# Performance work log

Measured on AMD Instinct MI355X. Metric: run time of the kernel, lower is better.

Reference implementation:

```python
import jax, jax.numpy as jnp
import numpy as np

D_MODEL = 1024
NUM_HEADS = 16
HEAD_DIM = D_MODEL // NUM_HEADS
ROPE_BASE = 10000.0


def setup_inputs() -> dict:
    key = jax.random.key(0)
    ks = jax.random.split(key, 9)
    B, S = 2, 2048
    x = jax.random.normal(ks[0], (B, S, D_MODEL), dtype=jnp.float32)
    s = 1.0 / np.sqrt(D_MODEL)
    Wq = jax.random.normal(ks[1], (D_MODEL, D_MODEL), dtype=jnp.float32) * s
    bq = jnp.zeros((D_MODEL,), dtype=jnp.float32)
    Wk = jax.random.normal(ks[2], (D_MODEL, D_MODEL), dtype=jnp.float32) * s
    bk = jnp.zeros((D_MODEL,), dtype=jnp.float32)
    Wv = jax.random.normal(ks[3], (D_MODEL, D_MODEL), dtype=jnp.float32) * s
    bv = jnp.zeros((D_MODEL,), dtype=jnp.float32)
    Wo = jax.random.normal(ks[4], (D_MODEL, D_MODEL), dtype=jnp.float32) * s
    bo = jnp.zeros((D_MODEL,), dtype=jnp.float32)
    return {"x": x, "Wq": Wq, "bq": bq, "Wk": Wk, "bk": bk,
            "Wv": Wv, "bv": bv, "Wo": Wo, "bo": bo}


def _apply_rope(x):
    # x: [B, H, S, Dh]; interleaved complex-pair RoPE (torch.view_as_complex style)
    B, H, S, Dh = x.shape
    inv_freq = 1.0 / (ROPE_BASE ** (jnp.arange(0, Dh, 2, dtype=jnp.float32) / Dh))
    pos = jnp.arange(S, dtype=jnp.float32)
    freqs = pos[:, None] * inv_freq[None, :]            # [S, Dh/2]
    cos, sin = jnp.cos(freqs), jnp.sin(freqs)           # each [S, Dh/2]
    x2 = x.reshape(B, H, S, Dh // 2, 2)
    xr, xi = x2[..., 0], x2[..., 1]
    out_r = xr * cos - xi * sin
    out_i = xr * sin + xi * cos
    return jnp.stack([out_r, out_i], axis=-1).reshape(B, H, S, Dh)


def reference(x, Wq, bq, Wk, bk, Wv, bv, Wo, bo):
    B, S, _ = x.shape
    H, Dh = NUM_HEADS, HEAD_DIM
    def proj(W, b):
        y = jnp.einsum('bsd,ed->bse', x, W) + b          # torch Linear: x @ W.T + b
        return y.reshape(B, S, H, Dh).transpose(0, 2, 1, 3)  # [B,H,S,Dh]
    Q = _apply_rope(proj(Wq, bq))
    K = _apply_rope(proj(Wk, bk))
    V = proj(Wv, bv)
    scale = 1.0 / jnp.sqrt(jnp.float32(Dh))
    scores = jnp.einsum('bhqd,bhkd->bhqk', Q, K) * scale
    causal = jnp.tril(jnp.ones((S, S), dtype=bool))
    scores = jnp.where(causal, scores, jnp.float32(-jnp.inf))
    attn = jax.nn.softmax(scores, axis=-1)
    out = jnp.einsum('bhqk,bhkd->bhqd', attn, V)         # [B,H,S,Dh]
    out = out.transpose(0, 2, 1, 3).reshape(B, S, H * Dh)
    return jnp.einsum('bsd,ed->bse', out, Wo) + bo
```

## Files before the change

### kernel.cpp

```cpp
#include <hip/hip_runtime.h>
#include <stdint.h>

#define S_LEN 2048
#define BATCH 2
#define DM 1024
#define NH 16
#define DH 64
#define MROWS 4096

typedef unsigned short u16;
typedef unsigned int u32;
typedef __attribute__((ext_vector_type(8))) short bf16x8;
typedef __attribute__((ext_vector_type(4))) short bf16x4;
typedef __attribute__((ext_vector_type(4))) float f32x4;
typedef __attribute__((ext_vector_type(2))) unsigned u32x2;

union pack8 { u32 w[4]; bf16x8 v8; };

__device__ inline u16 f2bf(float f) {
  union { float f; unsigned u; } v; v.f = f;
  unsigned u = v.u;
  unsigned r = u + 0x7fffu + ((u >> 16) & 1u);
  return (u16)(r >> 16);
}

__device__ inline u32 pkbf(float lo, float hi) {
  u32 r;
  asm("v_cvt_pk_bf16_f32 %0, %1, %2" : "=v"(r) : "v"(lo), "v"(hi));
  return r;
}

__global__ void convert_k(const float* __restrict__ x, const float* __restrict__ wq,
                          const float* __restrict__ wk, const float* __restrict__ wv,
                          const float* __restrict__ wo, u16* __restrict__ xb,
                          u16* __restrict__ wb) {
  int i = blockIdx.x * blockDim.x + threadIdx.x;
  const int total = (MROWS * DM + 4 * DM * DM) / 4;
  if (i >= total) return;
  int e = i * 4;
  const float* src;
  u16* dst;
  if (e < MROWS * DM) {
    src = x + e; dst = xb + e;
  } else {
    int j = e - MROWS * DM;
    int w = j >> 20;
    int o = j & ((1 << 20) - 1);
    src = (w == 0) ? wq + o : (w == 1) ? wk + o : (w == 2) ? wv + o : wo + o;
    dst = wb + j;
  }
  float4 v = *(const float4*)src;
  uint2 r;
  r.x = (unsigned)f2bf(v.x) | ((unsigned)f2bf(v.y) << 16);
  r.y = (unsigned)f2bf(v.z) | ((unsigned)f2bf(v.w) << 16);
  *(uint2*)dst = r;
}

__global__ void rope_k(float2* __restrict__ tab) {
  int i = blockIdx.x * blockDim.x + threadIdx.x;
  if (i >= S_LEN * 32) return;
  int s = i >> 5, p = i & 31;
  float inv = expf(-(float)p * 0.28782313662425575f);
  float a = (float)s * inv;
  tab[i] = make_float2(cosf(a), sinf(a));
}

__launch_bounds__(256)
__global__ void gemm_k(const u16* __restrict__ A,
                       const u16* __restrict__ w0, const u16* __restrict__ w1,
                       const u16* __restrict__ w2,
                       const float* __restrict__ b0, const float* __restrict__ b1,
                       const float* __restrict__ b2,
                       const float2* __restrict__ rope,
                       void* __restrict__ o0, void* __restrict__ o1, void* __restrict__ o2,
                       int mode0) {
  const int mode = mode0 + (int)(blockIdx.x >> 8);
  const int tile = blockIdx.x & 255;
  const int mt = tile >> 3, nt = tile & 7;
  const int mbase = mt * 128, nbase = nt * 128;
  const u16* W = (mode == 1) ? w1 : (mode == 2) ? w2 : w0;
  const float* bias = (mode == 1) ? b1 : (mode == 2) ? b2 : b0;
  void* outp = (mode == 1) ? o1 : (mode == 2) ? o2 : o0;

  __shared__ u16 As[128 * 40];
  __shared__ u16 Bs[128 * 40];

  const int t = threadIdx.x;
  const int lane = t & 63, wvi = t >> 6;
  const int lr = lane & 15, lg = lane >> 4;
  const int wm = (wvi >> 1) * 64, wn = (wvi & 1) * 64;

  f32x4 acc[4][4] = {};
  const int srow = t >> 2;
  const int scol = (t & 3) * 8;

  for (int kk = 0; kk < DM; kk += 32) {
    bf16x8 a0 = *(const bf16x8*)(A + (size_t)(mbase + srow) * DM + kk + scol);
    bf16x8 a1 = *(const bf16x8*)(A + (size_t)(mbase + 64 + srow) * DM + kk + scol);
    bf16x8 g0 = *(const bf16x8*)(W + (size_t)(nbase + srow) * DM + kk + scol);
    bf16x8 g1 = *(const bf16x8*)(W + (size_t)(nbase + 64 + srow) * DM + kk + scol);
    __syncthreads();
    *(bf16x8*)&As[srow * 40 + scol] = a0;
    *(bf16x8*)&As[(64 + srow) * 40 + scol] = a1;
    *(bf16x8*)&Bs[srow * 40 + scol] = g0;
    *(bf16x8*)&Bs[(64 + srow) * 40 + scol] = g1;
    __syncthreads();
    bf16x8 af[4], bfr[4];
#pragma unroll
    for (int mi = 0; mi < 4; mi++)
      af[mi] = *(const bf16x8*)&As[(wm + mi * 16 + lr) * 40 + lg * 8];
#pragma unroll
    for (int ni = 0; ni < 4; ni++)
      bfr[ni] = *(const bf16x8*)&Bs[(wn + ni * 16 + lr) * 40 + lg * 8];
#pragma unroll
    for (int mi = 0; mi < 4; mi++)
#pragma unroll
      for (int ni = 0; ni < 4; ni++)
        acc[mi][ni] = __builtin_amdgcn_mfma_f32_16x16x32_bf16(af[mi], bfr[ni], acc[mi][ni], 0, 0, 0);
  }

#pragma unroll
  for (int ni = 0; ni < 4; ni++) {
    const int col = nbase + wn + ni * 16 + lr;
    const float bv = bias[col];
#pragma unroll
    for (int mi = 0; mi < 4; mi++) {
      const int row0 = mbase + wm + mi * 16 + lg * 4;
      f32x4 v = acc[mi][ni];
#pragma unroll
      for (int r = 0; r < 4; r++) {
        float val = v[r] + bv;
        const int row = row0 + r;
        if (mode <= 1) {
          float nb = __shfl_xor(val, 1);
          const int d = col & 63, p = d >> 1, s = row & (S_LEN - 1);
          float2 cs = rope[s * 32 + p];
          float ov = (d & 1) ? (nb * cs.y + val * cs.x) : (val * cs.x - nb * cs.y);
          if (mode == 0) ov *= 0.18033688011112042f;
          const int b = row >> 11, h = col >> 6;
          ((u16*)outp)[((size_t)(b * NH + h) * S_LEN + s) * DH + d] = f2bf(ov);
        } else if (mode == 2) {
          const int b = row >> 11, h = col >> 6, d = col & 63, s = row & (S_LEN - 1);
          const int j = s & 31;
          const int pos = (s & ~31) + (((j & 15) >> 2) << 3) + ((j >> 4) << 2) + (j & 3);
          ((u16*)outp)[((size_t)(b * NH + h) * DH + d) * S_LEN + pos] = f2bf(val);
        } else {
          ((float*)outp)[(size_t)row * DM + col] = val;
        }
      }
    }
  }
}

__device__ __forceinline__ void sm_pv(const float a[8], float& m, float& l,
                                      bf16x8 v0, bf16x8 v1, bf16x8 v2, bf16x8 v3,
                                      f32x4* o) {
  float mx = fmaxf(fmaxf(fmaxf(a[0], a[1]), fmaxf(a[2], a[3])),
                   fmaxf(fmaxf(a[4], a[5]), fmaxf(a[6], a[7])));
  mx = fmaxf(mx, __shfl_xor(mx, 16));
  mx = fmaxf(mx, __shfl_xor(mx, 32));
  const float mn = fmaxf(m, mx);
  const float c = __builtin_amdgcn_exp2f(m - mn);
  m = mn;
  float p[8];
#pragma unroll
  for (int r = 0; r < 8; r++) p[r] = __builtin_amdgcn_exp2f(a[r] - mn);
  l = l * c + (((p[0] + p[1]) + (p[2] + p[3])) + ((p[4] + p[5]) + (p[6] + p[7])));
  pack8 pu;
  pu.w[0] = pkbf(p[0], p[1]);
  pu.w[1] = pkbf(p[2], p[3]);
  pu.w[2] = pkbf(p[4], p[5]);
  pu.w[3] = pkbf(p[6], p[7]);
#pragma unroll
  for (int i = 0; i < 4; i++)
#pragma unroll
    for (int r = 0; r < 4; r++) o[i * 2][r] *= c;
  o[0] = __builtin_amdgcn_mfma_f32_16x16x32_bf16(v0, pu.v8, o[0], 0, 0, 0);
  o[2] = __builtin_amdgcn_mfma_f32_16x16x32_bf16(v1, pu.v8, o[2], 0, 0, 0);
  o[4] = __builtin_amdgcn_mfma_f32_16x16x32_bf16(v2, pu.v8, o[4], 0, 0, 0);
  o[6] = __builtin_amdgcn_mfma_f32_16x16x32_bf16(v3, pu.v8, o[6], 0, 0, 0);
}

__launch_bounds__(128)
__global__ void attn_k(const u16* __restrict__ Q, const u16* __restrict__ K,
                       const u16* __restrict__ Vt, u16* __restrict__ Oo) {
  const int bh = blockIdx.x & 31;
  const int pr = blockIdx.x >> 5;
  const int wv = threadIdx.x >> 6;
  const int lane = threadIdx.x & 63;
  const int lr = lane & 15, lg = lane >> 4;
  const int tile = 63 - (pr * 2 + wv);
  const int qbase = tile * 32;

  const size_t qoff = ((size_t)bh * S_LEN + qbase + lr) * DH + lg * 8;
  const bf16x8 qA0 = *(const bf16x8*)(Q + qoff);
  const bf16x8 qA1 = *(const bf16x8*)(Q + qoff + 32);
  const bf16x8 qB0 = *(const bf16x8*)(Q + qoff + 16 * DH);
  const bf16x8 qB1 = *(const bf16x8*)(Q + qoff + 16 * DH + 32);

  f32x4 o[8] = {};
  float mA = -__builtin_inff(), mB = -__builtin_inff(), lA = 0.f, lB = 0.f;
  const f32x4 zero = {};
  const int nst = tile + 1;

  const u16* Kp = K + ((size_t)bh * S_LEN + lr) * DH + lg * 8;
  const u16* Vp = Vt + ((size_t)bh * DH + lr) * S_LEN + lg * 8;
  bf16x8 kc0 = *(const bf16x8*)(Kp);
  bf16x8 kc1 = *(const bf16x8*)(Kp + 32);
  bf16x8 kc2 = *(const bf16x8*)(Kp + 16 * DH);
  bf16x8 kc3 = *(const bf16x8*)(Kp + 16 * DH + 32);

  for (int it = 0; it < nst - 1; ++it) {
    bf16x8 v0 = *(const bf16x8*)(Vp);
    bf16x8 v1 = *(const bf16x8*)(Vp + 16 * S_LEN);
    bf16x8 v2 = *(const bf16x8*)(Vp + 32 * S_LEN);
    bf16x8 v3 = *(const bf16x8*)(Vp + 48 * S_LEN);
    Vp += 32;

    f32x4 sA0 = __builtin_amdgcn_mfma_f32_16x16x32_bf16(kc0, qA0, zero, 0, 0, 0);
    sA0 = __builtin_amdgcn_mfma_f32_16x16x32_bf16(kc1, qA1, sA0, 0, 0, 0);
    f32x4 sA1 = __builtin_amdgcn_mfma_f32_16x16x32_bf16(kc2, qA0, zero, 0, 0, 0);
    sA1 = __builtin_amdgcn_mfma_f32_16x16x32_bf16(kc3, qA1, sA1, 0, 0, 0);
    f32x4 sB0 = __builtin_amdgcn_mfma_f32_16x16x32_bf16(kc0, qB0, zero, 0, 0, 0);
    sB0 = __builtin_amdgcn_mfma_f32_16x16x32_bf16(kc1, qB1, sB0, 0, 0, 0);
    f32x4 sB1 = __builtin_amdgcn_mfma_f32_16x16x32_bf16(kc2, qB0, zero, 0, 0, 0);
    sB1 = __builtin_amdgcn_mfma_f32_16x16x32_bf16(kc3, qB1, sB1, 0, 0, 0);

    Kp += 32 * DH;
    kc0 = *(const bf16x8*)(Kp);
    kc1 = *(const bf16x8*)(Kp + 32);
    kc2 = *(const bf16x8*)(Kp + 16 * DH);
    kc3 = *(const bf16x8*)(Kp + 16 * DH + 32);

    float aA[8], aB[8];
#pragma unroll
    for (int r = 0; r < 4; r++) {
      aA[r] = sA0[r]; aA[4 + r] = sA1[r];
      aB[r] = sB0[r]; aB[4 + r] = sB1[r];
    }
    sm_pv(aA, mA, lA, v0, v1, v2, v3, &o[0]);
    sm_pv(aB, mB, lB, v0, v1, v2, v3, &o[1]);
  }

  {
    bf16x8 v0 = *(const bf16x8*)(Vp);
    bf16x8 v1 = *(const bf16x8*)(Vp + 16 * S_LEN);
    bf16x8 v2 = *(const bf16x8*)(Vp + 32 * S_LEN);
    bf16x8 v3 = *(const bf16x8*)(Vp + 48 * S_LEN);

    f32x4 sA0 = __builtin_amdgcn_mfma_f32_16x16x32_bf16(kc0, qA0, zero, 0, 0, 0);
    sA0 = __builtin_amdgcn_mfma_f32_16x16x32_bf16(kc1, qA1, sA0, 0, 0, 0);
    f32x4 sA1 = __builtin_amdgcn_mfma_f32_16x16x32_bf16(kc2, qA0, zero, 0, 0, 0);
    sA1 = __builtin_amdgcn_mfma_f32_16x16x32_bf16(kc3, qA1, sA1, 0, 0, 0);
    f32x4 sB0 = __builtin_amdgcn_mfma_f32_16x16x32_bf16(kc0, qB0, zero, 0, 0, 0);
    sB0 = __builtin_amdgcn_mfma_f32_16x16x32_bf16(kc1, qB1, sB0, 0, 0, 0);
    f32x4 sB1 = __builtin_amdgcn_mfma_f32_16x16x32_bf16(kc2, qB0, zero, 0, 0, 0);
    sB1 = __builtin_amdgcn_mfma_f32_16x16x32_bf16(kc3, qB1, sB1, 0, 0, 0);

    const int qrelA = lr - lg * 4;
    const int qrelB = qrelA + 16;
    float aA[8], aB[8];
#pragma unroll
    for (int r = 0; r < 4; r++) {
      aA[r]     = (r <= qrelA)      ? sA0[r] : -__builtin_inff();
      aA[4 + r] = (r + 16 <= qrelA) ? sA1[r] : -__builtin_inff();
      aB[r]     = sB0[r];
      aB[4 + r] = (r + 16 <= qrelB) ? sB1[r] : -__builtin_inff();
    }
    sm_pv(aA, mA, lA, v0, v1, v2, v3, &o[0]);
    sm_pv(aB, mB, lB, v0, v1, v2, v3, &o[1]);
  }

  lA += __shfl_xor(lA, 16); lA += __shfl_xor(lA, 32);
  lB += __shfl_xor(lB, 16); lB += __shfl_xor(lB, 32);
  const float rlA = __builtin_amdgcn_rcpf(lA);
  const float rlB = __builtin_amdgcn_rcpf(lB);

  const int b = bh >> 4, h = bh & 15;
  const size_t obaseA = ((size_t)b * S_LEN + qbase + lr) * DM + h * DH;
  const size_t obaseB = obaseA + (size_t)16 * DM;
#pragma unroll
  for (int dt = 0; dt < 4; dt++) {
    u32x2 pkA, pkB;
    pkA.x = pkbf(o[dt * 2][0] * rlA, o[dt * 2][1] * rlA);
    pkA.y = pkbf(o[dt * 2][2] * rlA, o[dt * 2][3] * rlA);
    pkB.x = pkbf(o[dt * 2 + 1][0] * rlB, o[dt * 2 + 1][1] * rlB);
    pkB.y = pkbf(o[dt * 2 + 1][2] * rlB, o[dt * 2 + 1][3] * rlB);
    *(u32x2*)(Oo + obaseA + dt * 16 + lg * 4) = pkA;
    *(u32x2*)(Oo + obaseB + dt * 16 + lg * 4) = pkB;
  }
}

extern "C" void kernel_launch(void* const* d_in, const int* in_sizes, int n_in,
                              void* d_out, int out_size, void* d_ws, size_t ws_size,
                              hipStream_t stream) {
  const float* x  = (const float*)d_in[0];
  const float* Wq = (const float*)d_in[1];
  const float* bq = (const float*)d_in[2];
  const float* Wk = (const float*)d_in[3];
  const float* bk = (const float*)d_in[4];
  const float* Wv = (const float*)d_in[5];
  const float* bv = (const float*)d_in[6];
  const float* Wo = (const float*)d_in[7];
  const float* bo = (const float*)d_in[8];

  char* ws = (char*)d_ws;
  u16* xb    = (u16*)(ws);
  u16* wb    = (u16*)(ws + (8u << 20));
  u16* Qb    = (u16*)(ws + (16u << 20));
  u16* Kb    = (u16*)(ws + (24u << 20));
  u16* Vtb   = (u16*)(ws + (32u << 20));
  u16* AOb   = (u16*)(ws + (40u << 20));
  float2* rt = (float2*)(ws + (48u << 20));

  convert_k<<<8192, 256, 0, stream>>>(x, Wq, Wk, Wv, Wo, xb, wb);
  rope_k<<<256, 256, 0, stream>>>(rt);
  gemm_k<<<768, 256, 0, stream>>>(xb, wb, wb + (1u << 20), wb + (2u << 20),
                                  bq, bk, bv, rt, Qb, Kb, Vtb, 0);
  attn_k<<<1024, 128, 0, stream>>>(Qb, Kb, Vtb, AOb);
  gemm_k<<<256, 256, 0, stream>>>(AOb, wb + (3u << 20), wb + (3u << 20), wb + (3u << 20),
                                  bo, bo, bo, rt, d_out, d_out, d_out, 3);
}
```

Baseline: 168.5 us.

## Replace online softmax max with static Cauchy-Schwarz bound from query and key norms

A new kernel computes each head's maximum key norm with atomics. The attention kernel then bounds every score by |q|·max|k| and uses that fixed value as the softmax shift. This removes the per-step running max, its cross-lane shuffles and the rescaling of the output accumulators. The attention launch also changes from two waves per block to one wave per block. The static shift is mathematically equivalent, but if the bound sits far above the real scores, exp2 can underflow and lose precision or give a zero denominator for larger-magnitude inputs.

```diff
diff --git a/kernel.cpp b/kernel.cpp
--- a/kernel.cpp
+++ b/kernel.cpp
@@ -11,7 +11,6 @@
 typedef unsigned short u16;
 typedef unsigned int u32;
 typedef __attribute__((ext_vector_type(8))) short bf16x8;
-typedef __attribute__((ext_vector_type(4))) short bf16x4;
 typedef __attribute__((ext_vector_type(4))) float f32x4;
 typedef __attribute__((ext_vector_type(2))) unsigned u32x2;
 
@@ -28,6 +27,11 @@
   u32 r;
   asm("v_cvt_pk_bf16_f32 %0, %1, %2" : "=v"(r) : "v"(lo), "v"(hi));
   return r;
+}
+
+__device__ inline float bf2f(short s) {
+  union { u32 u; float f; } c; c.u = ((u32)(u16)s) << 16;
+  return c.f;
 }
 
 __global__ void convert_k(const float* __restrict__ x, const float* __restrict__ wq,
@@ -56,13 +60,32 @@
   *(uint2*)dst = r;
 }
 
-__global__ void rope_k(float2* __restrict__ tab) {
+__global__ void rope_k(float2* __restrict__ tab, float* __restrict__ kmax) {
   int i = blockIdx.x * blockDim.x + threadIdx.x;
+  if (i < 32) kmax[i] = 0.f;
   if (i >= S_LEN * 32) return;
   int s = i >> 5, p = i & 31;
   float inv = expf(-(float)p * 0.28782313662425575f);
   float a = (float)s * inv;
   tab[i] = make_float2(cosf(a), sinf(a));
+}
+
+__global__ void knorm_k(const u16* __restrict__ K, float* __restrict__ kmax) {
+  const int row = blockIdx.x * 256 + threadIdx.x;
+  const int bh = row >> 11;
+  const u16* p = K + (size_t)row * DH;
+  float ss = 0.f;
+#pragma unroll
+  for (int i = 0; i < 8; i++) {
+    bf16x8 v = *(const bf16x8*)(p + i * 8);
+#pragma unroll
+    for (int j = 0; j < 8; j++) { float f = bf2f(v[j]); ss += f * f; }
+  }
+  float kn = sqrtf(ss);
+#pragma unroll
+  for (int d = 1; d < 64; d <<= 1) kn = fmaxf(kn, __shfl_xor(kn, d));
+  if ((threadIdx.x & 63) == 0)
+    atomicMax((unsigned*)(kmax + bh), __float_as_uint(kn));
 }
 
 __launch_bounds__(256)
@@ -152,45 +175,33 @@
   }
 }
 
-__device__ __forceinline__ void sm_pv(const float a[8], float& m, float& l,
-                                      bf16x8 v0, bf16x8 v1, bf16x8 v2, bf16x8 v3,
-                                      f32x4* o) {
-  float mx = fmaxf(fmaxf(fmaxf(a[0], a[1]), fmaxf(a[2], a[3])),
-                   fmaxf(fmaxf(a[4], a[5]), fmaxf(a[6], a[7])));
-  mx = fmaxf(mx, __shfl_xor(mx, 16));
-  mx = fmaxf(mx, __shfl_xor(mx, 32));
-  const float mn = fmaxf(m, mx);
-  const float c = __builtin_amdgcn_exp2f(m - mn);
-  m = mn;
+__device__ __forceinline__ void sm_pv_static(const float a[8], float m, float& l,
+                                             bf16x8 v0, bf16x8 v1, bf16x8 v2, bf16x8 v3,
+                                             f32x4* o) {
   float p[8];
 #pragma unroll
-  for (int r = 0; r < 8; r++) p[r] = __builtin_amdgcn_exp2f(a[r] - mn);
-  l = l * c + (((p[0] + p[1]) + (p[2] + p[3])) + ((p[4] + p[5]) + (p[6] + p[7])));
+  for (int r = 0; r < 8; r++) p[r] = __builtin_amdgcn_exp2f(a[r] - m);
+  l += ((p[0] + p[1]) + (p[2] + p[3])) + ((p[4] + p[5]) + (p[6] + p[7]));
   pack8 pu;
   pu.w[0] = pkbf(p[0], p[1]);
   pu.w[1] = pkbf(p[2], p[3]);
   pu.w[2] = pkbf(p[4], p[5]);
   pu.w[3] = pkbf(p[6], p[7]);
-#pragma unroll
-  for (int i = 0; i < 4; i++)
-#pragma unroll
-    for (int r = 0; r < 4; r++) o[i * 2][r] *= c;
   o[0] = __builtin_amdgcn_mfma_f32_16x16x32_bf16(v0, pu.v8, o[0], 0, 0, 0);
   o[2] = __builtin_amdgcn_mfma_f32_16x16x32_bf16(v1, pu.v8, o[2], 0, 0, 0);
   o[4] = __builtin_amdgcn_mfma_f32_16x16x32_bf16(v2, pu.v8, o[4], 0, 0, 0);
   o[6] = __builtin_amdgcn_mfma_f32_16x16x32_bf16(v3, pu.v8, o[6], 0, 0, 0);
 }
 
-__launch_bounds__(128)
+__launch_bounds__(64)
 __global__ void attn_k(const u16* __restrict__ Q, const u16* __restrict__ K,
-                       const u16* __restrict__ Vt, u16* __restrict__ Oo) {
+                       const u16* __restrict__ Vt, u16* __restrict__ Oo,
+                       const float* __restrict__ kmax) {
   const int bh = blockIdx.x & 31;
-  const int pr = blockIdx.x >> 5;
-  const int wv = threadIdx.x >> 6;
-  const int lane = threadIdx.x & 63;
+  const int tile = 63 - (blockIdx.x >> 5);
+  const int qbase = tile * 32;
+  const int lane = threadIdx.x;
   const int lr = lane & 15, lg = lane >> 4;
-  const int tile = 63 - (pr * 2 + wv);
-  const int qbase = tile * 32;
 
   const size_t qoff = ((size_t)bh * S_LEN + qbase + lr) * DH + lg * 8;
   const bf16x8 qA0 = *(const bf16x8*)(Q + qoff);
@@ -198,8 +209,22 @@
   const bf16x8 qB0 = *(const bf16x8*)(Q + qoff + 16 * DH);
   const bf16x8 qB1 = *(const bf16x8*)(Q + qoff + 16 * DH + 32);
 
+  float ssA = 0.f, ssB = 0.f;
+#pragma unroll
+  for (int j = 0; j < 8; j++) {
+    float a0 = bf2f(qA0[j]), a1 = bf2f(qA1[j]);
+    float b0 = bf2f(qB0[j]), b1 = bf2f(qB1[j]);
+    ssA += a0 * a0 + a1 * a1;
+    ssB += b0 * b0 + b1 * b1;
+  }
+  ssA += __shfl_xor(ssA, 16); ssA += __shfl_xor(ssA, 32);
+  ssB += __shfl_xor(ssB, 16); ssB += __shfl_xor(ssB, 32);
+  const float kmx = kmax[bh];
+  const float mA = sqrtf(ssA) * kmx;
+  const float mB = sqrtf(ssB) * kmx;
+
   f32x4 o[8] = {};
-  float mA = -__builtin_inff(), mB = -__builtin_inff(), lA = 0.f, lB = 0.f;
+  float lA = 0.f, lB = 0.f;
   const f32x4 zero = {};
   const int nst = tile + 1;
 
@@ -238,8 +263,8 @@
       aA[r] = sA0[r]; aA[4 + r] = sA1[r];
       aB[r] = sB0[r]; aB[4 + r] = sB1[r];
     }
-    sm_pv(aA, mA, lA, v0, v1, v2, v3, &o[0]);
-    sm_pv(aB, mB, lB, v0, v1, v2, v3, &o[1]);
+    sm_pv_static(aA, mA, lA, v0, v1, v2, v3, &o[0]);
+    sm_pv_static(aB, mB, lB, v0, v1, v2, v3, &o[1]);
   }
 
   {
@@ -267,8 +292,8 @@
       aB[r]     = sB0[r];
       aB[4 + r] = (r + 16 <= qrelB) ? sB1[r] : -__builtin_inff();
     }
-    sm_pv(aA, mA, lA, v0, v1, v2, v3, &o[0]);
-    sm_pv(aB, mB, lB, v0, v1, v2, v3, &o[1]);
+    sm_pv_static(aA, mA, lA, v0, v1, v2, v3, &o[0]);
+    sm_pv_static(aB, mB, lB, v0, v1, v2, v3, &o[1]);
   }
 
   lA += __shfl_xor(lA, 16); lA += __shfl_xor(lA, 32);
@@ -312,12 +337,14 @@
   u16* Vtb   = (u16*)(ws + (32u << 20));
   u16* AOb   = (u16*)(ws + (40u << 20));
   float2* rt = (float2*)(ws + (48u << 20));
+  float* kmx = (float*)(ws + (48u << 20) + (512u << 10));
 
   convert_k<<<8192, 256, 0, stream>>>(x, Wq, Wk, Wv, Wo, xb, wb);
-  rope_k<<<256, 256, 0, stream>>>(rt);
+  rope_k<<<256, 256, 0, stream>>>(rt, kmx);
   gemm_k<<<768, 256, 0, stream>>>(xb, wb, wb + (1u << 20), wb + (2u << 20),
                                   bq, bk, bv, rt, Qb, Kb, Vtb, 0);
-  attn_k<<<1024, 128, 0, stream>>>(Qb, Kb, Vtb, AOb);
+  knorm_k<<<256, 256, 0, stream>>>(Kb, kmx);
+  attn_k<<<2048, 64, 0, stream>>>(Qb, Kb, Vtb, AOb, kmx);
   gemm_k<<<256, 256, 0, stream>>>(AOb, wb + (3u << 20), wb + (3u << 20), wb + (3u << 20),
                                   bo, bo, bo, rt, d_out, d_out, d_out, 3);
 }
```

New measurement: 171.1 us. No clear change (+1.5%).
